# Kernel tuning notes

Measured on AMD Instinct MI355X. Metric: run time of the kernel, lower is better.

Reference implementation:

```python
import jax, jax.numpy as jnp
import numpy as np
import math

B, S, D, H, F, E, K, L, V = 1, 2048, 768, 12, 1536, 8, 2, 2, 32000


def _ln(x, w, b, eps=1e-5):
    m = x.mean(-1, keepdims=True)
    v = ((x - m) ** 2).mean(-1, keepdims=True)
    return (x - m) / jnp.sqrt(v + eps) * w + b


def setup_inputs() -> dict:
    key = jax.random.key(0)
    ks = jax.random.split(key, 16)
    std = 0.02
    inp = {
        'tokens': jax.random.randint(ks[0], (B, S), 0, V),
        'emb': jax.random.normal(ks[1], (V, D), jnp.float32) * std,
        'qkv_w': jax.random.normal(ks[2], (L, 3 * D, D), jnp.float32) * std,
        'qkv_b': jax.random.normal(ks[3], (L, 3 * D), jnp.float32) * std,
        'out_w': jax.random.normal(ks[4], (L, D, D), jnp.float32) * std,
        'out_b': jax.random.normal(ks[5], (L, D), jnp.float32) * std,
        'ln1_w': jnp.ones((L, D), jnp.float32),
        'ln1_b': jax.random.normal(ks[6], (L, D), jnp.float32) * std,
        'ln2_w': jnp.ones((L, D), jnp.float32),
        'ln2_b': jax.random.normal(ks[7], (L, D), jnp.float32) * std,
        'gate_w': jax.random.normal(ks[8], (L, E, D), jnp.float32) * std,
        'eg_w': jax.random.normal(ks[9], (L, E, F, D), jnp.float32) * std,
        'eu_w': jax.random.normal(ks[10], (L, E, F, D), jnp.float32) * std,
        'ed_w': jax.random.normal(ks[11], (L, E, D, F), jnp.float32) * std,
        'rms_w': jnp.ones((D,), jnp.float32),
    }
    return inp


def reference(tokens, emb, qkv_w, qkv_b, out_w, out_b, ln1_w, ln1_b,
              ln2_w, ln2_b, gate_w, eg_w, eu_w, ed_w, rms_w):
    Dh = D // H
    x = emb[tokens] * math.sqrt(D)  # (B,S,D)
    for l in range(L):
        # --- MultiheadAttention (batch_first, no mask, eval) ---
        qkv = x @ qkv_w[l].T + qkv_b[l]
        q, k, v = jnp.split(qkv, 3, axis=-1)
        q = q.reshape(B, S, H, Dh).transpose(0, 2, 1, 3)
        k = k.reshape(B, S, H, Dh).transpose(0, 2, 1, 3)
        v = v.reshape(B, S, H, Dh).transpose(0, 2, 1, 3)
        att = jax.nn.softmax(jnp.einsum('bhqd,bhkd->bhqk', q, k) / math.sqrt(Dh), axis=-1)
        o = jnp.einsum('bhqk,bhkd->bhqd', att, v).transpose(0, 2, 1, 3).reshape(B, S, D)
        o = o @ out_w[l].T + out_b[l]
        x = _ln(x + o, ln1_w[l], ln1_b[l])
        # --- SimpleDeepseekV3MoE: top-k gate, softmax over top-k scores ---
        gs = jnp.einsum('bsd,ed->bse', x, gate_w[l])
        topv, topi = jax.lax.top_k(gs, K)
        tw = jax.nn.softmax(topv, axis=-1)  # (B,S,K)
        # dense per-expert combine weight (0 for unselected experts)
        ew = jnp.sum(jax.nn.one_hot(topi, E, dtype=x.dtype) * tw[..., None], axis=-2)  # (B,S,E)
        hg = jax.nn.silu(jnp.einsum('bsd,efd->bsef', x, eg_w[l]))
        hu = jnp.einsum('bsd,efd->bsef', x, eu_w[l])
        ye = jnp.einsum('bsef,edf->bsed', hg * hu, ed_w[l])
        moe = jnp.einsum('bsed,bse->bsd', ye, ew)
        x = _ln(x + moe, ln2_w[l], ln2_b[l])
    # final RMSNorm (torch default eps=None -> finfo eps)
    rms = jnp.sqrt(jnp.mean(x * x, axis=-1, keepdims=True) + jnp.finfo(x.dtype).eps)
    x = x / rms * rms_w
    logits = x @ emb.T  # tied lm_head
    return logits
```

## Files before the change

kernel.cpp:

```cpp
#include <hip/hip_runtime.h>

#define SQ   2048
#define DM   768
#define NHD  12
#define DHD  64
#define FF   1536
#define NE   8
#define NL   2
#define NV   32000

typedef __attribute__((ext_vector_type(8))) short bf16x8;
typedef __attribute__((ext_vector_type(4))) float f32x4;

__device__ __forceinline__ unsigned short f2bf(float f) {
  unsigned u = __float_as_uint(f);
  return (unsigned short)((u + 0x7fffu + ((u >> 16) & 1u)) >> 16);
}
__device__ __forceinline__ float bf2f(unsigned short h) {
  return __uint_as_float(((unsigned)h) << 16);
}

#define GLD16(ldsp, gp) __builtin_amdgcn_global_load_lds( \
    (const __attribute__((address_space(1))) void*)(gp),  \
    (__attribute__((address_space(3))) void*)(ldsp), 16, 0, 0)

__device__ __forceinline__ void conv8(const float* s, unsigned short* d) {
  float4 a = *(const float4*)s;
  float4 b = *(const float4*)(s + 4);
  int4 pk = make_int4(
      (int)((unsigned)f2bf(a.x) | ((unsigned)f2bf(a.y) << 16)),
      (int)((unsigned)f2bf(a.z) | ((unsigned)f2bf(a.w) << 16)),
      (int)((unsigned)f2bf(b.x) | ((unsigned)f2bf(b.y) << 16)),
      (int)((unsigned)f2bf(b.z) | ((unsigned)f2bf(b.w) << 16)));
  *(int4*)d = pk;
}

__global__ __launch_bounds__(256) void conv_k(const float* __restrict__ s,
    unsigned short* __restrict__ d) {
  size_t i = (size_t)(blockIdx.x * 256 + threadIdx.x) * 8;
  conv8(s + i, d + i);
}

__global__ __launch_bounds__(256) void conv3_k(const float* __restrict__ s0,
    const float* __restrict__ s1, const float* __restrict__ s2,
    unsigned short* __restrict__ d, int per) {
  int b = blockIdx.x;
  const float* s = (b < per) ? s0 : (b < 2 * per) ? s1 : s2;
  int sb = (b < per) ? b : (b < 2 * per) ? b - per : b - 2 * per;
  size_t di = (size_t)b * 2048 + threadIdx.x * 8;
  size_t si = (size_t)sb * 2048 + threadIdx.x * 8;
  conv8(s + si, d + di);
}

__global__ __launch_bounds__(256) void conv2_k(const float* __restrict__ s0,
    const float* __restrict__ s1, unsigned short* __restrict__ d, int per0) {
  int b = blockIdx.x;
  const float* s = (b < per0) ? s0 : s1;
  int sb = (b < per0) ? b : b - per0;
  size_t di = (size_t)b * 2048 + threadIdx.x * 8;
  size_t si = (size_t)sb * 2048 + threadIdx.x * 8;
  conv8(s + si, d + di);
}

__global__ __launch_bounds__(256) void embed_k(const int* __restrict__ tok,
    const float* __restrict__ emb, float* __restrict__ x,
    unsigned short* __restrict__ xbf) {
  int idx = blockIdx.x * 256 + threadIdx.x;
  int s = idx / DM, d = idx % DM;
  float v = emb[(size_t)tok[s] * DM + d] * 27.712812921102035f;
  x[idx] = v;
  xbf[idx] = f2bf(v);
}

__global__ __launch_bounds__(256, 2) void gemm8s_k(
    const unsigned short* __restrict__ A, long long lda,
    const unsigned short* __restrict__ B, long long ldb,
    float* __restrict__ C, long long ldc,
    int Kd, int mT)
{
  int nwg = gridDim.x, bid = blockIdx.x;
  int q = nwg >> 3, r = nwg & 7;
  int xcd = bid & 7, j = bid >> 3;
  int wid = (xcd < r ? xcd * (q + 1) : r * (q + 1) + (xcd - r) * q) + j;
  int mt = wid % mT, nt = wid / mT;
  int m0 = mt * 128, n0 = nt * 128;

  __shared__ __align__(16) unsigned short lds[2][2][8192];

  int t = threadIdx.x, w = t >> 6, lane = t & 63;
  int wm = w >> 1, wn = w & 1;
  int fr = lane & 15, ksg = lane >> 4;
  int lchunk = ((lane & 7) ^ (lane >> 3)) * 8;

  const unsigned short* sa[4];
  const unsigned short* sb[4];
  #pragma unroll
  for (int i = 0; i < 4; ++i) {
    sa[i] = A + (size_t)(m0 + i * 32 + w * 8 + (lane >> 3)) * lda + lchunk;
    sb[i] = B + (size_t)(n0 + i * 32 + w * 8 + (lane >> 3)) * ldb + lchunk;
  }

  int KT = Kd >> 6;
  f32x4 acc[4][4] = {};

#define STAGE_A8(bufi, k0) { _Pragma("unroll") \
    for (int i = 0; i < 4; ++i) \
      GLD16(&lds[bufi][0][(i * 32 + w * 8) * 64], sa[i] + (k0)); }
#define STAGE_B8(bufi, k0) { _Pragma("unroll") \
    for (int i = 0; i < 4; ++i) \
      GLD16(&lds[bufi][1][(i * 32 + w * 8) * 64], sb[i] + (k0)); }

  STAGE_A8(0, 0); STAGE_B8(0, 0);
  asm volatile("s_waitcnt vmcnt(0)" ::: "memory");
  __builtin_amdgcn_s_barrier();
  __builtin_amdgcn_sched_barrier(0);

  int buf = 0;
  for (int kt = 0; kt < KT; ++kt) {
    const unsigned short* Al = &lds[buf][0][0];
    const unsigned short* Bl = &lds[buf][1][0];
    int pf = (kt + 1 < KT);
    long long koff = (long long)(kt + 1) * 64;
    bf16x8 afr[4], bfr[4];
    #pragma unroll
    for (int ph = 0; ph < 2; ++ph) {
      int ko = ((ph * 4 + ksg) ^ (fr & 7)) * 8;
      #pragma unroll
      for (int m = 0; m < 4; ++m)
        afr[m] = *(const bf16x8*)&Al[(wm * 64 + m * 16 + fr) * 64 + ko];
      #pragma unroll
      for (int n = 0; n < 4; ++n)
        bfr[n] = *(const bf16x8*)&Bl[(wn * 64 + n * 16 + fr) * 64 + ko];
      if (pf) {
        if (ph == 0) { STAGE_A8(buf ^ 1, koff); }
        else         { STAGE_B8(buf ^ 1, koff); }
      }
      __builtin_amdgcn_s_barrier();
      asm volatile("s_waitcnt lgkmcnt(0)" ::: "memory");
      __builtin_amdgcn_sched_barrier(0);
      __builtin_amdgcn_s_setprio(1);
      #pragma unroll
      for (int m = 0; m < 4; ++m)
        #pragma unroll
        for (int n = 0; n < 4; ++n)
          acc[m][n] = __builtin_amdgcn_mfma_f32_16x16x32_bf16(
              afr[m], bfr[n], acc[m][n], 0, 0, 0);
      __builtin_amdgcn_s_setprio(0);
      if (ph == 1 && pf) asm volatile("s_waitcnt vmcnt(0)" ::: "memory");
      __builtin_amdgcn_s_barrier();
      __builtin_amdgcn_sched_barrier(0);
    }
    buf ^= 1;
  }
#undef STAGE_A8
#undef STAGE_B8

  int rb = ksg * 4;
  #pragma unroll
  for (int m = 0; m < 4; ++m)
    #pragma unroll
    for (int n = 0; n < 4; ++n)
      #pragma unroll
      for (int rr = 0; rr < 4; ++rr)
        C[(size_t)(m0 + wm * 64 + m * 16 + rb + rr) * ldc +
          (n0 + wn * 64 + n * 16 + fr)] = acc[m][n][rr];
}

template<bool GATHER, bool OBF16>
__global__ __launch_bounds__(512) void gemm256_k(
    const unsigned short* __restrict__ A, long long lda,
    const unsigned short* __restrict__ B, long long ldb, long long b_z,
    void* __restrict__ C, long long ldc, long long c_z,
    int M, int Kd, int mT, int nT, int Z, int zmod,
    const int* __restrict__ glist, long long gl_z,
    const int* __restrict__ cnt)
{
  int nwg = gridDim.x, bid = blockIdx.x;
  int q = nwg >> 3, r = nwg & 7;
  int xcd = bid & 7, j = bid >> 3;
  int wid = (xcd < r ? xcd * (q + 1) : r * (q + 1) + (xcd - r) * q) + j;
  int z = wid % Z; int rem = wid / Z;
  int mt = rem % mT, nt = rem / mT;
  int zz = z % zmod;
  int Mz = cnt ? cnt[zz] : M;
  int m0 = mt * 128, n0 = nt * 256;
  if (m0 >= Mz) return;
  (void)nT;

  const unsigned short* Bz = B + (size_t)z * b_z;

  __shared__ __align__(16) unsigned short lds[3 * 6 * 4096];

  int t = threadIdx.x, w = t >> 6, lane = t & 63;
  int wm = (w >> 2) * 64, wn = (w & 3) * 64;
  int fr = lane & 15, ksg = lane >> 4;
  int lrow = lane >> 3;
  int lchunk = ((lane & 7) ^ lrow) * 8;

  const unsigned short* sp[6];
  #pragma unroll
  for (int hh = 0; hh < 2; ++hh) {
    int gr = m0 + hh * 64 + w * 8 + lrow; if (gr >= Mz) gr = Mz - 1;
    int arow;
    if constexpr (GATHER) arow = glist[(size_t)zz * gl_z + gr]; else arow = gr;
    sp[hh] = A + (size_t)arow * lda + lchunk;
  }
  #pragma unroll
  for (int hh = 0; hh < 4; ++hh)
    sp[2 + hh] = Bz + (size_t)(n0 + hh * 64 + w * 8 + lrow) * ldb + lchunk;

  int rdA = (w >> 2) * 4096;
  int rdB = (2 + (w & 3)) * 4096;
  int stDst = w * 512;

  int rx = fr & 7;
  int off0 = (ksg ^ rx) * 8;
  int off1 = ((4 + ksg) ^ rx) * 8;

  int KT = Kd >> 6;
  f32x4 acc[4][4] = {};

  #pragma unroll
  for (int h = 0; h < 6; ++h)
    GLD16(&lds[h * 4096 + stDst], sp[h]);
  #pragma unroll
  for (int h = 0; h < 6; ++h)
    GLD16(&lds[(6 + h) * 4096 + stDst], sp[h] + 64);
  asm volatile("s_waitcnt vmcnt(6)" ::: "memory");
  __builtin_amdgcn_s_barrier();
  __builtin_amdgcn_sched_barrier(0);

  int buf = 0;
  for (int kt = 0; kt < KT; ++kt) {
    const unsigned short* Abl = &lds[buf * 6 * 4096 + rdA];
    const unsigned short* Bbl = &lds[buf * 6 * 4096 + rdB];
    int pf = (kt + 2 < KT);
    int pbuf = buf + 2; if (pbuf >= 3) pbuf -= 3;
    unsigned short* pd = &lds[pbuf * 6 * 4096 + stDst];
    long long koff = (long long)(kt + 2) * 64;

    if (pf) {
      GLD16(pd + 0 * 4096, sp[0] + koff);
      GLD16(pd + 1 * 4096, sp[1] + koff);
      GLD16(pd + 2 * 4096, sp[2] + koff);
    }
    {
      bf16x8 af[4], bv[4];
      #pragma unroll
      for (int m = 0; m < 4; ++m)
        af[m] = *(const bf16x8*)&Abl[(m * 16 + fr) * 64 + off0];
      #pragma unroll
      for (int n = 0; n < 4; ++n)
        bv[n] = *(const bf16x8*)&Bbl[(n * 16 + fr) * 64 + off0];
      __builtin_amdgcn_s_setprio(1);
      #pragma unroll
      for (int m = 0; m < 4; ++m)
        #pragma unroll
        for (int n = 0; n < 4; ++n)
          acc[m][n] = __builtin_amdgcn_mfma_f32_16x16x32_bf16(
              af[m], bv[n], acc[m][n], 0, 0, 0);
      __builtin_amdgcn_s_setprio(0);
    }
    if (pf) {
      GLD16(pd + 3 * 4096, sp[3] + koff);
      GLD16(pd + 4 * 4096, sp[4] + koff);
      GLD16(pd + 5 * 4096, sp[5] + koff);
    }
    {
      bf16x8 af[4], bv[4];
      #pragma unroll
      for (int m = 0; m < 4; ++m)
        af[m] = *(const bf16x8*)&Abl[(m * 16 + fr) * 64 + off1];
      #pragma unroll
      for (int n = 0; n < 4; ++n)
        bv[n] = *(const bf16x8*)&Bbl[(n * 16 + fr) * 64 + off1];
      __builtin_amdgcn_s_setprio(1);
      #pragma unroll
      for (int m = 0; m < 4; ++m)
        #pragma unroll
        for (int n = 0; n < 4; ++n)
          acc[m][n] = __builtin_amdgcn_mfma_f32_16x16x32_bf16(
              af[m], bv[n], acc[m][n], 0, 0, 0);
      __builtin_amdgcn_s_setprio(0);
    }
    if (pf) {
      asm volatile("s_waitcnt vmcnt(6)" ::: "memory");
    } else if (kt + 1 < KT) {
      asm volatile("s_waitcnt vmcnt(0)" ::: "memory");
    }
    __builtin_amdgcn_s_barrier();
    __builtin_amdgcn_sched_barrier(0);
    buf = buf + 1; if (buf == 3) buf = 0;
  }

  int rb = ksg * 4;
  #pragma unroll
  for (int m = 0; m < 4; ++m) {
    #pragma unroll
    for (int n = 0; n < 4; ++n) {
      #pragma unroll
      for (int rr = 0; rr < 4; ++rr) {
        int row = m0 + wm + m * 16 + rb + rr;
        if (row >= Mz) continue;
        size_t off = (size_t)z * c_z + (size_t)row * ldc +
                     (n0 + wn + n * 16 + fr);
        if constexpr (OBF16) ((unsigned short*)C)[off] = f2bf(acc[m][n][rr]);
        else                 ((float*)C)[off] = acc[m][n][rr];
      }
    }
  }
}

template<bool GATHER, bool BIAS, bool OBF16, bool VT>
__global__ __launch_bounds__(256) void gemm_k(
    const unsigned short* __restrict__ A, long long lda, long long a_z,
    const unsigned short* __restrict__ B, long long ldb, long long b_z,
    const float* __restrict__ bias,
    void* __restrict__ C, long long ldc, long long c_z,
    int M, int N, int Kd, float scale,
    const int* __restrict__ glist, long long gl_z,
    const int* __restrict__ cnt, int mT, int nT, int Z,
    unsigned short* __restrict__ vtout)
{
  int nwg = gridDim.x, bid = blockIdx.x;
  int q = nwg >> 3, r = nwg & 7;
  int xcd = bid & 7, j = bid >> 3;
  int wid = (xcd < r ? xcd * (q + 1) : r * (q + 1) + (xcd - r) * q) + j;
  int z = wid % Z; int rem = wid / Z;
  int mt = rem % mT, nt = rem / mT;

  int Mz = cnt ? cnt[z] : M;
  int m0 = mt * 128, n0 = nt * 128;
  if (m0 >= Mz) return;

  const unsigned short* Ab = A + (size_t)z * a_z;
  const unsigned short* Bb = B + (size_t)z * b_z;

  __shared__ __align__(16) unsigned short As[128 * 64];
  __shared__ __align__(16) unsigned short Bs[128 * 64];

  int t = threadIdx.x, w = t >> 6, lane = t & 63;
  int wm = (w >> 1) * 64, wn = (w & 1) * 64;
  int fr = lane & 15, ksg = lane >> 4;
  int lrow = lane >> 3;
  int lchunk = ((lane & 7) ^ lrow) * 8;

  const unsigned short* ap[4];
  const unsigned short* bp[4];
  unsigned short* la[4];
  unsigned short* lb[4];
  #pragma unroll
  for (int i = 0; i < 4; ++i) {
    int rrow = w * 32 + i * 8 + lrow;
    int gr = m0 + rrow; if (gr >= Mz) gr = Mz - 1;
    int arow; if constexpr (GATHER) arow = glist[(size_t)z * gl_z + gr]; else arow = gr;
    ap[i] = Ab + (size_t)arow * lda + lchunk;
    int br = n0 + rrow; if (br >= N) br = N - 1;
    bp[i] = Bb + (size_t)br * ldb + lchunk;
    la[i] = &As[(w * 32 + i * 8) * 64];
    lb[i] = &Bs[(w * 32 + i * 8) * 64];
  }

  int rx = fr & 7;
  int off0 = ((0 + ksg) ^ rx) * 8;
  int off1 = ((4 + ksg) ^ rx) * 8;

  f32x4 acc[4][4] = {};

  for (int k0 = 0; k0 < Kd; k0 += 64) {
    #pragma unroll
    for (int i = 0; i < 4; ++i) GLD16(la[i], ap[i] + k0);
    #pragma unroll
    for (int i = 0; i < 4; ++i) GLD16(lb[i], bp[i] + k0);
    __syncthreads();
    #pragma unroll
    for (int kb = 0; kb < 2; ++kb) {
      int offk = kb ? off1 : off0;
      bf16x8 af[4], bv[4];
      #pragma unroll
      for (int m = 0; m < 4; ++m)
        af[m] = *(const bf16x8*)&As[(wm + m * 16 + fr) * 64 + offk];
      #pragma unroll
      for (int n = 0; n < 4; ++n)
        bv[n] = *(const bf16x8*)&Bs[(wn + n * 16 + fr) * 64 + offk];
      #pragma unroll
      for (int m = 0; m < 4; ++m)
        #pragma unroll
        for (int n = 0; n < 4; ++n)
          acc[m][n] = __builtin_amdgcn_mfma_f32_16x16x32_bf16(
              af[m], bv[n], acc[m][n], 0, 0, 0);
    }
    __syncthreads();
  }

  int rb = ksg * 4;
  #pragma unroll
  for (int m = 0; m < 4; ++m) {
    #pragma unroll
    for (int n = 0; n < 4; ++n) {
      int col = n0 + wn + n * 16 + fr;
      if (col >= N) continue;
      #pragma unroll
      for (int rr = 0; rr < 4; ++rr) {
        int row = m0 + wm + m * 16 + rb + rr;
        if (row >= Mz) continue;
        float v = acc[m][n][rr] * scale;
        if constexpr (BIAS) v += bias[col];
        size_t off = (size_t)z * c_z + (size_t)row * ldc + col;
        if constexpr (OBF16) ((unsigned short*)C)[off] = f2bf(v);
        else                 ((float*)C)[off] = v;
        if constexpr (VT) {
          if (n0 >= 2 * DM)
            vtout[(size_t)(col - 2 * DM) * SQ + row] = f2bf(v);
        }
      }
    }
  }
}

__global__ __launch_bounds__(128) void flash_k(
    const unsigned short* __restrict__ qkv,
    const unsigned short* __restrict__ vt,
    unsigned short* __restrict__ o)
{
  int nwg = gridDim.x, bid = blockIdx.x;
  int cpx = nwg >> 3;
  int wid = (bid & 7) * cpx + (bid >> 3);
  int h  = wid >> 6;
  int qt = wid & 63;
  int q0 = qt * 32;

  __shared__ __align__(16) unsigned short Ks[128 * 64];
  __shared__ __align__(16) unsigned short Vs[128 * 64];
  __shared__ __align__(16) unsigned short Ps[2][16 * 136];

  int t = threadIdx.x, w = t >> 6, lane = t & 63;
  int fr = lane & 15, ksg = lane >> 4;
  int lrow = lane >> 3;
  int lchunk = ((lane & 7) ^ lrow) * 8;

  const unsigned short* qbase = qkv + (size_t)q0 * (3 * DM) + h * DHD;
  #pragma unroll
  for (int i = 0; i < 2; ++i) {
    int rrow = w * 16 + i * 8 + lrow;
    GLD16(&Ks[(w * 16 + i * 8) * 64], qbase + (size_t)rrow * (3 * DM) + lchunk);
  }
  __syncthreads();
  bf16x8 qf[2];
  {
    int row = w * 16 + fr, ph = fr & 7;
    qf[0] = *(const bf16x8*)&Ks[row * 64 + ((ksg ^ ph) * 8)];
    qf[1] = *(const bf16x8*)&Ks[row * 64 + (((4 + ksg) ^ ph) * 8)];
  }
  __syncthreads();

  const unsigned short* kbase = qkv + DM + h * DHD;
  const unsigned short* vb = vt + (size_t)(h * DHD) * SQ;

  f32x4 oacc[4] = {};
  float m_r[4] = {-1e30f, -1e30f, -1e30f, -1e30f};
  float l_r[4] = {0.f, 0.f, 0.f, 0.f};

  for (int kt = 0; kt < SQ / 128; ++kt) {
    int kk0 = kt * 128;
    #pragma unroll
    for (int i = 0; i < 8; ++i) {
      int rrow = w * 64 + i * 8 + lrow;
      GLD16(&Ks[(w * 64 + i * 8) * 64],
            kbase + (size_t)(kk0 + rrow) * (3 * DM) + lchunk);
    }
    #pragma unroll
    for (int i = 0; i < 8; ++i) {
      int p = w * 64 + i * 8 + lrow;
      GLD16(&Vs[(w * 64 + i * 8) * 64],
            vb + (size_t)(p >> 1) * SQ + kk0 + (p & 1) * 64 + lchunk);
    }
    __syncthreads();

    f32x4 sacc[8] = {};
    #pragma unroll
    for (int kb = 0; kb < 2; ++kb) {
      #pragma unroll
      for (int n = 0; n < 8; ++n) {
        int row = n * 16 + fr;
        bf16x8 bvv = *(const bf16x8*)&Ks[row * 64 +
            (((kb * 4 + ksg) ^ (fr & 7)) * 8)];
        sacc[n] = __builtin_amdgcn_mfma_f32_16x16x32_bf16(
            qf[kb], bvv, sacc[n], 0, 0, 0);
      }
    }

    #pragma unroll
    for (int r = 0; r < 4; ++r) {
      float mx = sacc[0][r];
      #pragma unroll
      for (int n = 1; n < 8; ++n) mx = fmaxf(mx, sacc[n][r]);
      mx = fmaxf(mx, __shfl_xor(mx, 1));
      mx = fmaxf(mx, __shfl_xor(mx, 2));
      mx = fmaxf(mx, __shfl_xor(mx, 4));
      mx = fmaxf(mx, __shfl_xor(mx, 8));
      float mn = fmaxf(m_r[r], mx * 0.125f);
      float resc = __expf(m_r[r] - mn);
      m_r[r] = mn;
      #pragma unroll
      for (int n = 0; n < 4; ++n) oacc[n][r] *= resc;
      float rs = 0.f;
      #pragma unroll
      for (int n = 0; n < 8; ++n) {
        float p = __expf(sacc[n][r] * 0.125f - mn);
        rs += p;
        Ps[w][(ksg * 4 + r) * 136 + n * 16 + fr] = f2bf(p);
      }
      rs += __shfl_xor(rs, 1);
      rs += __shfl_xor(rs, 2);
      rs += __shfl_xor(rs, 4);
      rs += __shfl_xor(rs, 8);
      l_r[r] = l_r[r] * resc + rs;
    }

    #pragma unroll
    for (int ksi = 0; ksi < 4; ++ksi) {
      bf16x8 pa = *(const bf16x8*)&Ps[w][fr * 136 + ksi * 32 + ksg * 8];
      #pragma unroll
      for (int n = 0; n < 4; ++n) {
        int p = (n * 16 + fr) * 2 + (ksi >> 1);
        int c = (ksi & 1) * 4 + ksg;
        bf16x8 bvv = *(const bf16x8*)&Vs[p * 64 + ((c ^ (p & 7)) * 8)];
        oacc[n] = __builtin_amdgcn_mfma_f32_16x16x32_bf16(
            pa, bvv, oacc[n], 0, 0, 0);
      }
    }
    __syncthreads();
  }

  unsigned short* ob = o + (size_t)(q0 + w * 16) * DM + h * DHD;
  #pragma unroll
  for (int r = 0; r < 4; ++r) {
    float invl = 1.f / l_r[r];
    int qrow = ksg * 4 + r;
    #pragma unroll
    for (int n = 0; n < 4; ++n)
      ob[(size_t)qrow * DM + n * 16 + fr] = f2bf(oacc[n][r] * invl);
  }
}

__global__ __launch_bounds__(256) void add_ln_gate_k(const float* __restrict__ xin,
    const float* __restrict__ add, const float* __restrict__ w,
    const float* __restrict__ b, const float* __restrict__ gw,
    float* __restrict__ xout, unsigned short* __restrict__ xbf,
    float* __restrict__ tw, int* __restrict__ ti, int* __restrict__ cnt,
    int* __restrict__ lists, int* __restrict__ slot) {
  int row = blockIdx.x, t = threadIdx.x;
  const float* xi = xin + (size_t)row * DM;
  const float* ai = add + (size_t)row * DM;
  float v[3]; float s = 0.f, sq = 0.f;
  #pragma unroll
  for (int i = 0; i < 3; ++i) {
    int idx = t + i * 256;
    v[i] = xi[idx] + ai[idx];
    s += v[i]; sq += v[i] * v[i];
  }
  #pragma unroll
  for (int o = 32; o; o >>= 1) { s += __shfl_xor(s, o); sq += __shfl_xor(sq, o); }
  __shared__ float rsm[4], rqm[4];
  __shared__ float gsm[4][NE];
  int wv = t >> 6, lane = t & 63;
  if (lane == 0) { rsm[wv] = s; rqm[wv] = sq; }
  __syncthreads();
  s = rsm[0] + rsm[1] + rsm[2] + rsm[3];
  sq = rqm[0] + rqm[1] + rqm[2] + rqm[3];
  float mean = s * (1.f / 768.f);
  float var = sq * (1.f / 768.f) - mean * mean;
  float inv = rsqrtf(var + 1e-5f);
  float* xo = xout + (size_t)row * DM;
  unsigned short* xb = xbf + (size_t)row * DM;
  float y[3];
  #pragma unroll
  for (int i = 0; i < 3; ++i) {
    int idx = t + i * 256;
    y[i] = (v[i] - mean) * inv * w[idx] + b[idx];
    xo[idx] = y[i]; xb[idx] = f2bf(y[i]);
  }
  float p[NE];
  #pragma unroll
  for (int e = 0; e < NE; ++e) {
    p[e] = y[0] * gw[e * DM + t] + y[1] * gw[e * DM + t + 256]
         + y[2] * gw[e * DM + t + 512];
    #pragma unroll
    for (int o = 32; o; o >>= 1) p[e] += __shfl_xor(p[e], o);
  }
  if (lane == 0) {
    #pragma unroll
    for (int e = 0; e < NE; ++e) gsm[wv][e] = p[e];
  }
  __syncthreads();
  if (t == 0) {
    float v0 = -1e30f, v1 = -1e30f; int i0 = 0, i1 = 0;
    #pragma unroll
    for (int e = 0; e < NE; ++e) {
      float g = gsm[0][e] + gsm[1][e] + gsm[2][e] + gsm[3][e];
      if (g > v0) { v1 = v0; i1 = i0; v0 = g; i0 = e; }
      else if (g > v1) { v1 = g; i1 = e; }
    }
    float e1 = expf(v1 - v0);
    float invs = 1.f / (1.f + e1);
    tw[row * 2] = invs; tw[row * 2 + 1] = e1 * invs;
    ti[row * 2] = i0;   ti[row * 2 + 1] = i1;
    int p0 = atomicAdd(&cnt[i0], 1); lists[i0 * SQ + p0] = row; slot[row * 2] = p0;
    int p1 = atomicAdd(&cnt[i1], 1); lists[i1 * SQ + p1] = row; slot[row * 2 + 1] = p1;
  }
}

__global__ void zero_k(int* __restrict__ c) {
  if (threadIdx.x < NE) c[threadIdx.x] = 0;
}

__global__ __launch_bounds__(256) void silu_mul_k(unsigned short* __restrict__ hg,
    const unsigned short* __restrict__ hu, const int* __restrict__ cnt) {
  int e = blockIdx.y, sl = blockIdx.x;
  if (sl >= cnt[e]) return;
  size_t base = ((size_t)e * SQ + sl) * FF;
  int t = threadIdx.x;
  #pragma unroll
  for (int i = 0; i < FF / 256; ++i) {
    size_t idx = base + t + i * 256;
    float g = bf2f(hg[idx]);
    float u = bf2f(hu[idx]);
    float sv = g / (1.f + expf(-g));
    hg[idx] = f2bf(sv * u);
  }
}

__global__ __launch_bounds__(256) void combine_ln_k(const float* __restrict__ xin,
    const float* __restrict__ ye, const float* __restrict__ tw,
    const int* __restrict__ ti, const int* __restrict__ slot,
    const float* __restrict__ w, const float* __restrict__ b,
    float* __restrict__ xout, unsigned short* __restrict__ xbf) {
  int row = blockIdx.x, t = threadIdx.x;
  int e0 = ti[row * 2], e1 = ti[row * 2 + 1];
  int p0 = slot[row * 2], p1 = slot[row * 2 + 1];
  float w0 = tw[row * 2], w1 = tw[row * 2 + 1];
  const float* y0 = ye + ((size_t)e0 * SQ + p0) * DM;
  const float* y1 = ye + ((size_t)e1 * SQ + p1) * DM;
  const float* xi = xin + (size_t)row * DM;
  float v[3]; float s = 0.f, sq = 0.f;
  #pragma unroll
  for (int i = 0; i < 3; ++i) {
    int idx = t + i * 256;
    v[i] = xi[idx] + w0 * y0[idx] + w1 * y1[idx];
    s += v[i]; sq += v[i] * v[i];
  }
  #pragma unroll
  for (int o = 32; o; o >>= 1) { s += __shfl_xor(s, o); sq += __shfl_xor(sq, o); }
  __shared__ float rsm[4], rqm[4];
  int wv = t >> 6;
  if ((t & 63) == 0) { rsm[wv] = s; rqm[wv] = sq; }
  __syncthreads();
  s = rsm[0] + rsm[1] + rsm[2] + rsm[3];
  sq = rqm[0] + rqm[1] + rqm[2] + rqm[3];
  float mean = s * (1.f / 768.f);
  float var = sq * (1.f / 768.f) - mean * mean;
  float inv = rsqrtf(var + 1e-5f);
  float* xo = xout + (size_t)row * DM;
  unsigned short* xb = xbf + (size_t)row * DM;
  #pragma unroll
  for (int i = 0; i < 3; ++i) {
    int idx = t + i * 256;
    float y = (v[i] - mean) * inv * w[idx] + b[idx];
    xo[idx] = y; xb[idx] = f2bf(y);
  }
}

__global__ __launch_bounds__(256) void rms_k(const float* __restrict__ x,
    const float* __restrict__ rw, unsigned short* __restrict__ xbf) {
  int row = blockIdx.x, t = threadIdx.x;
  const float* xi = x + (size_t)row * DM;
  float v[3]; float sq = 0.f;
  #pragma unroll
  for (int i = 0; i < 3; ++i) {
    int idx = t + i * 256;
    v[i] = xi[idx];
    sq += v[i] * v[i];
  }
  #pragma unroll
  for (int o = 32; o; o >>= 1) sq += __shfl_xor(sq, o);
  __shared__ float rqm[4];
  int wv = t >> 6;
  if ((t & 63) == 0) rqm[wv] = sq;
  __syncthreads();
  sq = rqm[0] + rqm[1] + rqm[2] + rqm[3];
  float inv = rsqrtf(sq * (1.f / 768.f) + 1.1920929e-07f);
  unsigned short* xb = xbf + (size_t)row * DM;
  #pragma unroll
  for (int i = 0; i < 3; ++i) {
    int idx = t + i * 256;
    xb[idx] = f2bf(v[i] * inv * rw[idx]);
  }
}

extern "C" void kernel_launch(void* const* d_in, const int* in_sizes, int n_in,
                              void* d_out, int out_size, void* d_ws, size_t ws_size,
                              hipStream_t stream) {
  (void)in_sizes; (void)n_in; (void)out_size; (void)ws_size;
  const int*   tokens = (const int*)d_in[0];
  const float* emb    = (const float*)d_in[1];
  const float* qkv_w  = (const float*)d_in[2];
  const float* qkv_b  = (const float*)d_in[3];
  const float* out_w  = (const float*)d_in[4];
  const float* out_b  = (const float*)d_in[5];
  const float* ln1_w  = (const float*)d_in[6];
  const float* ln1_b  = (const float*)d_in[7];
  const float* ln2_w  = (const float*)d_in[8];
  const float* ln2_b  = (const float*)d_in[9];
  const float* gate_w = (const float*)d_in[10];
  const float* eg_w   = (const float*)d_in[11];
  const float* eu_w   = (const float*)d_in[12];
  const float* ed_w   = (const float*)d_in[13];
  const float* rms_w  = (const float*)d_in[14];
  float* out = (float*)d_out;

  char* wsb = (char*)d_ws;
  float*          x_f    = (float*)(wsb + 0);
  unsigned short* x_bf   = (unsigned short*)(wsb + 6291456);
  unsigned short* qkv_bf = (unsigned short*)(wsb + 9437184);
  unsigned short* vt     = (unsigned short*)(wsb + 18874368);
  unsigned short* o_bf   = (unsigned short*)(wsb + 22020096);
  float*          tmp_f  = (float*)(wsb + 25165824);
  float*          tw     = (float*)(wsb + 31457280);
  int*            ti     = (int*)(wsb + 31473664);
  int*            cnt    = (int*)(wsb + 31490048);
  int*            lists  = (int*)(wsb + 31490304);
  int*            slot   = (int*)(wsb + 31555840);
  unsigned short* emb_bf = (unsigned short*)(wsb + 31572224);
  unsigned short* wbf    = (unsigned short*)(wsb + 80724224);
  unsigned short* hg     = (unsigned short*)(wsb + 142065920);
  unsigned short* hu     = (unsigned short*)(wsb + 142065920 + 50331648);
  float*          ye     = (float*)(wsb + 142065920 + 50331648);

  unsigned short* qw_bf = wbf;
  unsigned short* ow_bf = wbf + 1769472;
  unsigned short* eg_bf = wbf + 2359296;
  unsigned short* ed_bf = wbf + 21233664;

  conv_k<<<12000, 256, 0, stream>>>(emb, emb_bf);
  embed_k<<<SQ * DM / 256, 256, 0, stream>>>(tokens, emb, x_f, x_bf);

  for (int l = 0; l < NL; ++l) {
    const float* qw = qkv_w + (size_t)l * 3 * DM * DM;
    const float* qb = qkv_b + (size_t)l * 3 * DM;
    const float* ob = out_b + (size_t)l * DM;
    const float* ow = out_w + (size_t)l * DM * DM;
    const float* gw = gate_w + (size_t)l * NE * DM;
    const float* egw = eg_w + (size_t)l * NE * FF * DM;
    const float* euw = eu_w + (size_t)l * NE * FF * DM;
    const float* edw = ed_w + (size_t)l * NE * DM * FF;

    conv2_k<<<1152, 256, 0, stream>>>(qw, ow, qw_bf, 864);
    conv3_k<<<13824, 256, 0, stream>>>(egw, euw, edw, eg_bf, 4608);

    gemm_k<false, true, true, true><<<16 * 18, 256, 0, stream>>>(
        x_bf, DM, 0, qw_bf, DM, 0, qb, qkv_bf, 3 * DM, 0,
        SQ, 3 * DM, DM, 1.f, nullptr, 0, nullptr, 16, 18, 1, vt);

    flash_k<<<NHD * 64, 128, 0, stream>>>(qkv_bf, vt, o_bf);

    gemm_k<false, true, false, false><<<16 * 6, 256, 0, stream>>>(
        o_bf, DM, 0, ow_bf, DM, 0, ob, tmp_f, DM, 0,
        SQ, DM, DM, 1.f, nullptr, 0, nullptr, 16, 6, 1, nullptr);

    zero_k<<<1, 64, 0, stream>>>(cnt);
    add_ln_gate_k<<<SQ, 256, 0, stream>>>(x_f, tmp_f, ln1_w + l * DM,
        ln1_b + l * DM, gw, x_f, x_bf, tw, ti, cnt, lists, slot);

    gemm256_k<true, true><<<16 * 6 * 16, 512, 0, stream>>>(
        x_bf, DM, eg_bf, DM, (long long)FF * DM,
        hg, FF, (long long)SQ * FF,
        SQ, DM, 16, 6, 16, 8, lists, SQ, cnt);

    silu_mul_k<<<dim3(SQ, NE), 256, 0, stream>>>(hg, hu, cnt);

    gemm_k<false, false, false, false><<<16 * 6 * NE, 256, 0, stream>>>(
        hg, FF, (long long)SQ * FF, ed_bf, FF, (long long)DM * FF, nullptr,
        ye, DM, (long long)SQ * DM,
        SQ, DM, FF, 1.f, nullptr, 0, cnt, 16, 6, NE, nullptr);

    combine_ln_k<<<SQ, 256, 0, stream>>>(x_f, ye, tw, ti, slot,
                                         ln2_w + l * DM, ln2_b + l * DM,
                                         x_f, x_bf);
  }

  rms_k<<<SQ, 256, 0, stream>>>(x_f, rms_w, x_bf);

  gemm8s_k<<<16 * 250, 256, 0, stream>>>(
      x_bf, DM, emb_bf, DM, out, NV, DM, 16);
}
```

Measured before the change: 828.7 us.

## Use 256x256 tiles with 4-stage LDS pipeline for lm_head GEMM

Replaces the 128x128 double-buffered lm_head GEMM with a 512-thread, 256x256-tile kernel that stages K in 32-wide slices through a 4-slot LDS ring with prefetch depth two. Larger tiles raise arithmetic intensity and reduce global reloads of A and B, while the deeper ring with vmcnt-based waits is meant to hide load latency with one barrier per step. It trades occupancy (one block per CU, 8x4 accumulators per wave) and leaves fewer workgroups (1000) to balance across CUs.

```diff
diff --git a/kernel.cpp b/kernel.cpp
--- a/kernel.cpp
+++ b/kernel.cpp
@@ -72,7 +72,7 @@
   xbf[idx] = f2bf(v);
 }
 
-__global__ __launch_bounds__(256, 2) void gemm8s_k(
+__global__ __launch_bounds__(512, 1) void gemmr_k(
     const unsigned short* __restrict__ A, long long lda,
     const unsigned short* __restrict__ B, long long ldb,
     float* __restrict__ C, long long ldc,
@@ -83,87 +83,80 @@
   int xcd = bid & 7, j = bid >> 3;
   int wid = (xcd < r ? xcd * (q + 1) : r * (q + 1) + (xcd - r) * q) + j;
   int mt = wid % mT, nt = wid / mT;
-  int m0 = mt * 128, n0 = nt * 128;
-
-  __shared__ __align__(16) unsigned short lds[2][2][8192];
+  int m0 = mt * 256, n0 = nt * 256;
+
+  __shared__ __align__(16) unsigned short lds[4][2][8192];
 
   int t = threadIdx.x, w = t >> 6, lane = t & 63;
-  int wm = w >> 1, wn = w & 1;
+  int wm = w >> 2, wn = w & 3;
   int fr = lane & 15, ksg = lane >> 4;
-  int lchunk = ((lane & 7) ^ (lane >> 3)) * 8;
-
-  const unsigned short* sa[4];
-  const unsigned short* sb[4];
-  #pragma unroll
-  for (int i = 0; i < 4; ++i) {
-    sa[i] = A + (size_t)(m0 + i * 32 + w * 8 + (lane >> 3)) * lda + lchunk;
-    sb[i] = B + (size_t)(n0 + i * 32 + w * 8 + (lane >> 3)) * ldb + lchunk;
-  }
-
-  int KT = Kd >> 6;
-  f32x4 acc[4][4] = {};
-
-#define STAGE_A8(bufi, k0) { _Pragma("unroll") \
-    for (int i = 0; i < 4; ++i) \
-      GLD16(&lds[bufi][0][(i * 32 + w * 8) * 64], sa[i] + (k0)); }
-#define STAGE_B8(bufi, k0) { _Pragma("unroll") \
-    for (int i = 0; i < 4; ++i) \
-      GLD16(&lds[bufi][1][(i * 32 + w * 8) * 64], sb[i] + (k0)); }
-
-  STAGE_A8(0, 0); STAGE_B8(0, 0);
-  asm volatile("s_waitcnt vmcnt(0)" ::: "memory");
+
+  int srow = t >> 2;
+  int schunk = ((t & 3) ^ (srow & 3)) * 8;
+  const unsigned short* sa0 = A + (size_t)(m0 +       srow) * lda + schunk;
+  const unsigned short* sa1 = A + (size_t)(m0 + 128 + srow) * lda + schunk;
+  const unsigned short* sb0 = B + (size_t)(n0 +       srow) * ldb + schunk;
+  const unsigned short* sb1 = B + (size_t)(n0 + 128 + srow) * ldb + schunk;
+  int wofs = w * 512;
+
+  int NS = Kd >> 5;
+  f32x4 acc[8][4] = {};
+
+#define STAGEV(s) { \
+    int sl_ = (s) & 3; \
+    long long ko_ = (long long)((s) >> 1) * 64 + ((s) & 1) * 32; \
+    GLD16(&lds[sl_][0][wofs], sa0 + ko_); \
+    GLD16(&lds[sl_][0][4096 + wofs], sa1 + ko_); \
+    GLD16(&lds[sl_][1][wofs], sb0 + ko_); \
+    GLD16(&lds[sl_][1][4096 + wofs], sb1 + ko_); }
+
+  STAGEV(0);
+  STAGEV(1);
+  asm volatile("s_waitcnt vmcnt(4)" ::: "memory");
   __builtin_amdgcn_s_barrier();
   __builtin_amdgcn_sched_barrier(0);
 
-  int buf = 0;
-  for (int kt = 0; kt < KT; ++kt) {
-    const unsigned short* Al = &lds[buf][0][0];
-    const unsigned short* Bl = &lds[buf][1][0];
-    int pf = (kt + 1 < KT);
-    long long koff = (long long)(kt + 1) * 64;
-    bf16x8 afr[4], bfr[4];
-    #pragma unroll
-    for (int ph = 0; ph < 2; ++ph) {
-      int ko = ((ph * 4 + ksg) ^ (fr & 7)) * 8;
-      #pragma unroll
-      for (int m = 0; m < 4; ++m)
-        afr[m] = *(const bf16x8*)&Al[(wm * 64 + m * 16 + fr) * 64 + ko];
+  int ko = (ksg ^ (fr & 3)) * 8;
+  for (int s = 0; s < NS; ++s) {
+    int slot = s & 3;
+    const unsigned short* Al = &lds[slot][0][0];
+    const unsigned short* Bl = &lds[slot][1][0];
+    bf16x8 af[8], bf[4];
+    #pragma unroll
+    for (int m = 0; m < 8; ++m)
+      af[m] = *(const bf16x8*)&Al[(wm * 128 + m * 16 + fr) * 32 + ko];
+    #pragma unroll
+    for (int n = 0; n < 4; ++n)
+      bf[n] = *(const bf16x8*)&Bl[(wn * 64 + n * 16 + fr) * 32 + ko];
+    if (s + 2 < NS) STAGEV(s + 2);
+    asm volatile("s_waitcnt lgkmcnt(0)" ::: "memory");
+    __builtin_amdgcn_sched_barrier(0);
+    __builtin_amdgcn_s_setprio(1);
+    #pragma unroll
+    for (int m = 0; m < 8; ++m)
       #pragma unroll
       for (int n = 0; n < 4; ++n)
-        bfr[n] = *(const bf16x8*)&Bl[(wn * 64 + n * 16 + fr) * 64 + ko];
-      if (pf) {
-        if (ph == 0) { STAGE_A8(buf ^ 1, koff); }
-        else         { STAGE_B8(buf ^ 1, koff); }
-      }
-      __builtin_amdgcn_s_barrier();
-      asm volatile("s_waitcnt lgkmcnt(0)" ::: "memory");
-      __builtin_amdgcn_sched_barrier(0);
-      __builtin_amdgcn_s_setprio(1);
-      #pragma unroll
-      for (int m = 0; m < 4; ++m)
-        #pragma unroll
-        for (int n = 0; n < 4; ++n)
-          acc[m][n] = __builtin_amdgcn_mfma_f32_16x16x32_bf16(
-              afr[m], bfr[n], acc[m][n], 0, 0, 0);
-      __builtin_amdgcn_s_setprio(0);
-      if (ph == 1 && pf) asm volatile("s_waitcnt vmcnt(0)" ::: "memory");
+        acc[m][n] = __builtin_amdgcn_mfma_f32_16x16x32_bf16(
+            af[m], bf[n], acc[m][n], 0, 0, 0);
+    __builtin_amdgcn_s_setprio(0);
+    if (s + 1 < NS) {
+      if (s + 2 < NS) asm volatile("s_waitcnt vmcnt(4)" ::: "memory");
+      else            asm volatile("s_waitcnt vmcnt(0)" ::: "memory");
       __builtin_amdgcn_s_barrier();
       __builtin_amdgcn_sched_barrier(0);
     }
-    buf ^= 1;
-  }
-#undef STAGE_A8
-#undef STAGE_B8
+  }
+#undef STAGEV
 
   int rb = ksg * 4;
   #pragma unroll
-  for (int m = 0; m < 4; ++m)
+  for (int M = 0; M < 8; ++M)
     #pragma unroll
     for (int n = 0; n < 4; ++n)
       #pragma unroll
       for (int rr = 0; rr < 4; ++rr)
-        C[(size_t)(m0 + wm * 64 + m * 16 + rb + rr) * ldc +
-          (n0 + wn * 64 + n * 16 + fr)] = acc[m][n][rr];
+        C[(size_t)(m0 + wm * 128 + M * 16 + rb + rr) * ldc +
+          (n0 + wn * 64 + n * 16 + fr)] = acc[M][n][rr];
 }
 
 template<bool GATHER, bool OBF16>
@@ -791,6 +784,6 @@
 
   rms_k<<<SQ, 256, 0, stream>>>(x_f, rms_w, x_bf);
 
-  gemm8s_k<<<16 * 250, 256, 0, stream>>>(
-      x_bf, DM, emb_bf, DM, out, NV, DM, 16);
-}
+  gemmr_k<<<8 * 125, 512, 0, stream>>>(
+      x_bf, DM, emb_bf, DM, out, NV, DM, 8);
+}
```

After: 794.1 us. 4.2% less time.
